# Kernel tuning notes

Hardware: AMD Instinct MI355X
Metric: run time of the kernel (lower is better)

Reference implementation:

```python
import jax, jax.numpy as jnp
import numpy as np

# Working config of MultiHeadAttention2d (see notes): B=1, k=1, n_heads=1,
# residual=True, channel_cross_attention=False, kernel_size=1.
# ConvNormActivation2d is modeled as a plain 1x1 Conv2d (bias=True for q/k/v,
# bias=False for the residual projection), i.e. identity norm/activation.
C = 64   # in_channels == out_channels == y_in == y_out (defaults, n_heads=1)
H = 36
W = 36
HW = H * W


def _conv1x1(t, Wm, b=None):
    # t: (1, C, H, W), Wm: (Cout, Cin)
    o = jnp.einsum('bchw,oc->bohw', t, Wm)
    if b is not None:
        o = o + b[None, :, None, None]
    return o


def setup_inputs() -> dict:
    key = jax.random.key(0)
    ks = jax.random.split(key, 10)
    s = 1.0 / np.sqrt(C).astype(np.float32)
    x = jax.random.normal(ks[0], (1, C, H, W), jnp.float32)
    y = jax.random.normal(ks[1], (1, C, H, W), jnp.float32)
    Wq = jax.random.normal(ks[2], (C, C), jnp.float32) * s
    bq = jnp.zeros((C,), jnp.float32)
    Wk = jax.random.normal(ks[3], (C, C), jnp.float32) * s
    bk = jnp.zeros((C,), jnp.float32)
    Wv = jax.random.normal(ks[4], (C, C), jnp.float32) * s
    bv = jnp.zeros((C,), jnp.float32)
    Wp = jax.random.normal(ks[5], (C, C), jnp.float32) * s  # residual projection, bias=False
    gamma = jax.random.uniform(ks[6], (1, 1, 1), jnp.float32) + 0.001  # torch.rand(...) + 0.001
    return {'x': x, 'y': y, 'Wq': Wq, 'bq': bq, 'Wk': Wk, 'bk': bk,
            'Wv': Wv, 'bv': bv, 'Wp': Wp, 'gamma': gamma}


def reference(x, y, Wq, bq, Wk, bk, Wv, bv, Wp, gamma):
    # 1x1-conv QKV projections
    q = _conv1x1(x, Wq, bq).reshape(C, HW)   # bmm batch dim is B*C = C (chxa=False)
    k = _conv1x1(x, Wk, bk).reshape(C, HW)
    v = _conv1x1(y, Wv, bv).reshape(C, HW)
    # energy = bmm(q^T, k) with inner dim k=1 -> per-channel outer product (C, HW, HW)
    energy = q[:, :, None] * k[:, None, :]
    att = jax.nn.softmax(energy, axis=-1)            # softmax over keys (last dim)
    # out = bmm(v, att^T): out[c,i] = sum_j v[c,j] * att[c,i,j]
    out = jnp.einsum('cij,cj->ci', att, v)           # (C, HW)
    # gamma-gated residual blend with projected y
    yproj = _conv1x1(y, Wp).reshape(C, HW)
    g = gamma.reshape(())                            # (1,1,1) gamma broadcasts as scalar
    out = (g * out + yproj) / (1.0 + g)
    return out.reshape(1, C, H, W)
```

## Files before the change

kernel.cpp:

```cpp
#include <hip/hip_runtime.h>
#include <math.h>

#define CCH 64
#define HWN 1296
#define NTHREADS 256
#define NTILES 21
#define TS 216
#define TT 6

#if defined(__has_builtin)
#  if __has_builtin(__builtin_amdgcn_exp2f)
#    define FAST_EXP2(x) __builtin_amdgcn_exp2f(x)
#  else
#    define FAST_EXP2(x) __expf((x) * 0.69314718055994531f)
#  endif
#else
#  define FAST_EXP2(x) __expf((x) * 0.69314718055994531f)
#endif

__global__ __launch_bounds__(NTHREADS) void proj2(
    const float* __restrict__ x, const float* __restrict__ y,
    const float* __restrict__ Wq, const float* __restrict__ bq,
    const float* __restrict__ Wk, const float* __restrict__ bk,
    const float* __restrict__ Wv, const float* __restrict__ bv,
    const float* __restrict__ Wp,
    float* __restrict__ q, float* __restrict__ k,
    float* __restrict__ v, float* __restrict__ yp)
{
    __shared__ float wsA[2][CCH], wsB[2][CCH];
    const int b = blockIdx.x;
    const bool xpart = (b < 324);
    const int bb = xpart ? b : b - 324;
    const int tid = threadIdx.x;
    const int idx = bb * NTHREADS + tid;
    const int c = idx / HWN;
    const int p = idx - c * HWN;
    const int c0 = (bb * NTHREADS) / HWN;
    const int c1 = (bb * NTHREADS + NTHREADS - 1) / HWN;

    {
        const int i6 = tid & 63;
        const int rsel = (tid >> 6) & 1;
        const int msel = tid >> 7;
        const int crow = rsel ? c1 : c0;
        const float* WA = xpart ? Wq : Wv;
        const float* WB = xpart ? Wk : Wp;
        if (msel == 0) wsA[rsel][i6] = WA[crow * CCH + i6];
        else           wsB[rsel][i6] = WB[crow * CCH + i6];
    }
    __syncthreads();

    const int rs = (c == c0) ? 0 : 1;
    const float* wA = wsA[rs];
    const float* wB = wsB[rs];
    float accA = xpart ? bq[c] : bv[c];
    float accB = xpart ? bk[c] : 0.f;
    const float* src = xpart ? x : y;
    const float* col = src + p;

    #pragma unroll
    for (int u = 0; u < CCH; u += 16) {
        float xv[16];
        #pragma unroll
        for (int t = 0; t < 16; ++t) xv[t] = col[(u + t) * HWN];
        #pragma unroll
        for (int t = 0; t < 16; ++t) {
            accA = fmaf(wA[u + t], xv[t], accA);
            accB = fmaf(wB[u + t], xv[t], accB);
        }
    }
    if (xpart) { q[idx] = accA; k[idx] = accB; }
    else       { v[idx] = accA; yp[idx] = accB; }
}

__global__ __launch_bounds__(NTHREADS) void att2(
    const float* __restrict__ q, const float* __restrict__ k,
    const float* __restrict__ v, const float* __restrict__ yp,
    const float* __restrict__ gamma, float* __restrict__ out)
{
    __shared__ __align__(16) float4 k4[HWN / 4];
    __shared__ __align__(16) float4 v4[HWN / 4];
    __shared__ float sse[4][64], ssev[4][64];
    __shared__ float swmax[4], swmin[4];
    const int c = blockIdx.x / NTILES;
    const int itile = blockIdx.x % NTILES;
    const int tid = threadIdx.x;
    const int w = tid >> 6;
    const int l = tid & 63;

    const float4* kg = (const float4*)(k + c * HWN);
    const float4* vg = (const float4*)(v + c * HWN);
    float lmax = -1e30f, lmin = 1e30f;
    for (int j = tid; j < HWN / 4; j += NTHREADS) {
        const float4 kk = kg[j];
        k4[j] = kk;
        v4[j] = vg[j];
        lmax = fmaxf(fmaxf(lmax, kk.x), fmaxf(kk.y, fmaxf(kk.z, kk.w)));
        lmin = fminf(fminf(lmin, kk.x), fminf(kk.y, fminf(kk.z, kk.w)));
    }
    #pragma unroll
    for (int off = 32; off > 0; off >>= 1) {
        lmax = fmaxf(lmax, __shfl_xor(lmax, off, 64));
        lmin = fminf(lmin, __shfl_xor(lmin, off, 64));
    }
    if (l == 0) { swmax[w] = lmax; swmin[w] = lmin; }
    __syncthreads();
    const float kmax = fmaxf(fmaxf(swmax[0], swmax[1]), fmaxf(swmax[2], swmax[3]));
    const float kmin = fminf(fminf(swmin[0], swmin[1]), fminf(swmin[2], swmin[3]));

    const int i = itile * 64 + l;
    const int iv = (i < HWN) ? i : (HWN - 1);
    const float L2E = 1.4426950408889634f;
    const float a2 = q[c * HWN + iv] * L2E;
    const float m2 = (a2 >= 0.f) ? a2 * kmax : a2 * kmin;
    float se = 0.f, sev = 0.f;
    const int j0 = w * 81;
    #pragma unroll 3
    for (int jj = 0; jj < 81; ++jj) {
        const float4 kk = k4[j0 + jj];
        const float4 vv = v4[j0 + jj];
        const float e0 = FAST_EXP2(fmaf(a2, kk.x, -m2));
        const float e1 = FAST_EXP2(fmaf(a2, kk.y, -m2));
        const float e2 = FAST_EXP2(fmaf(a2, kk.z, -m2));
        const float e3 = FAST_EXP2(fmaf(a2, kk.w, -m2));
        se += (e0 + e1) + (e2 + e3);
        sev = fmaf(e0, vv.x, sev);
        sev = fmaf(e1, vv.y, sev);
        sev = fmaf(e2, vv.z, sev);
        sev = fmaf(e3, vv.w, sev);
    }
    sse[w][l] = se;
    ssev[w][l] = sev;
    __syncthreads();
    if (tid < 64) {
        const int io = itile * 64 + tid;
        if (io < HWN) {
            const float seT  = (sse[0][tid] + sse[1][tid]) + (sse[2][tid] + sse[3][tid]);
            const float sevT = (ssev[0][tid] + ssev[1][tid]) + (ssev[2][tid] + ssev[3][tid]);
            const float g = gamma[0];
            out[c * HWN + io] = (g * (sevT / seT) + yp[c * HWN + io]) / (1.f + g);
        }
    }
}

__global__ __launch_bounds__(NTHREADS) void fused_kernel(
    const float* __restrict__ x, const float* __restrict__ y,
    const float* __restrict__ Wq, const float* __restrict__ bq,
    const float* __restrict__ Wk, const float* __restrict__ bk,
    const float* __restrict__ Wv, const float* __restrict__ bv,
    const float* __restrict__ Wp, const float* __restrict__ gamma,
    float* __restrict__ out)
{
    __shared__ __align__(16) float ks[HWN];
    __shared__ __align__(16) float vs[HWN];
    __shared__ float wq[CCH], wk[CCH], wv[CCH], wp[CCH];
    __shared__ float qs[TS], yps[TS];
    __shared__ float swmax[4], swmin[4];
    __shared__ float skmax, skmin;
    const int c = blockIdx.x / TT;
    const int t = blockIdx.x % TT;
    const int tid = threadIdx.x;

    if (tid < CCH) {
        wq[tid] = Wq[c * CCH + tid];
        wk[tid] = Wk[c * CCH + tid];
        wv[tid] = Wv[c * CCH + tid];
        wp[tid] = Wp[c * CCH + tid];
    }
    __syncthreads();
    const float bkc = bk[c], bvc = bv[c], bqc = bq[c];

    float lmax = -1e30f, lmin = 1e30f;
    for (int j = tid; j < HWN; j += NTHREADS) {
        float ak = bkc, av = bvc;
        #pragma unroll 8
        for (int i = 0; i < CCH; ++i) {
            ak = fmaf(wk[i], x[i * HWN + j], ak);
            av = fmaf(wv[i], y[i * HWN + j], av);
        }
        ks[j] = ak; vs[j] = av;
        lmax = fmaxf(lmax, ak);
        lmin = fminf(lmin, ak);
    }
    for (int ii = tid; ii < TS; ii += NTHREADS) {
        const int p = t * TS + ii;
        float aq = bqc, ap = 0.f;
        #pragma unroll 8
        for (int i = 0; i < CCH; ++i) {
            aq = fmaf(wq[i], x[i * HWN + p], aq);
            ap = fmaf(wp[i], y[i * HWN + p], ap);
        }
        qs[ii] = aq; yps[ii] = ap;
    }
    #pragma unroll
    for (int off = 32; off > 0; off >>= 1) {
        lmax = fmaxf(lmax, __shfl_xor(lmax, off, 64));
        lmin = fminf(lmin, __shfl_xor(lmin, off, 64));
    }
    const int wave = tid >> 6;
    if ((tid & 63) == 0) { swmax[wave] = lmax; swmin[wave] = lmin; }
    __syncthreads();
    if (tid == 0) {
        skmax = fmaxf(fmaxf(swmax[0], swmax[1]), fmaxf(swmax[2], swmax[3]));
        skmin = fminf(fminf(swmin[0], swmin[1]), fminf(swmin[2], swmin[3]));
    }
    __syncthreads();

    if (tid < TS) {
        const int i = t * TS + tid;
        const float L2E = 1.4426950408889634f;
        const float a2 = qs[tid] * L2E;
        const float m2 = (a2 >= 0.f) ? a2 * skmax : a2 * skmin;
        float se = 0.f, sev = 0.f;
        const float4* k4 = (const float4*)ks;
        const float4* v4 = (const float4*)vs;
        #pragma unroll 2
        for (int jj = 0; jj < HWN / 4; ++jj) {
            const float4 kk = k4[jj];
            const float4 vv = v4[jj];
            const float e0 = FAST_EXP2(fmaf(a2, kk.x, -m2));
            const float e1 = FAST_EXP2(fmaf(a2, kk.y, -m2));
            const float e2 = FAST_EXP2(fmaf(a2, kk.z, -m2));
            const float e3 = FAST_EXP2(fmaf(a2, kk.w, -m2));
            se += (e0 + e1) + (e2 + e3);
            sev = fmaf(e0, vv.x, sev);
            sev = fmaf(e1, vv.y, sev);
            sev = fmaf(e2, vv.z, sev);
            sev = fmaf(e3, vv.w, sev);
        }
        const float g = gamma[0];
        const float att = sev / se;
        out[c * HWN + i] = (g * att + yps[tid]) / (1.f + g);
    }
}

extern "C" void kernel_launch(void* const* d_in, const int* in_sizes, int n_in,
                              void* d_out, int out_size, void* d_ws, size_t ws_size,
                              hipStream_t stream) {
    (void)in_sizes; (void)n_in; (void)out_size;
    const float* x  = (const float*)d_in[0];
    const float* y  = (const float*)d_in[1];
    const float* Wq = (const float*)d_in[2];
    const float* bq = (const float*)d_in[3];
    const float* Wk = (const float*)d_in[4];
    const float* bk = (const float*)d_in[5];
    const float* Wv = (const float*)d_in[6];
    const float* bv = (const float*)d_in[7];
    const float* Wp = (const float*)d_in[8];
    const float* gamma = (const float*)d_in[9];
    float* out = (float*)d_out;

    const size_t need = (size_t)4 * CCH * HWN * sizeof(float);
    if (ws_size >= need) {
        float* q  = (float*)d_ws;
        float* k  = q + CCH * HWN;
        float* v  = k + CCH * HWN;
        float* yp = v + CCH * HWN;
        proj2<<<648, NTHREADS, 0, stream>>>(x, y, Wq, bq, Wk, bk, Wv, bv, Wp,
                                            q, k, v, yp);
        att2<<<CCH * NTILES, NTHREADS, 0, stream>>>(q, k, v, yp, gamma, out);
    } else {
        fused_kernel<<<CCH * TT, NTHREADS, 0, stream>>>(x, y, Wq, bq, Wk, bk, Wv, bv, Wp,
                                                        gamma, out);
    }
}
```

Measured before the change: 93.28 us.

## Process four query rows per thread in attention kernel to reuse K/V loads

The attention kernel now gives each thread up to four query positions (216-row tiles, 6 tiles per channel) instead of one per thread with 21 tiles per channel. Each LDS load of k/v float4 is reused across four rows, cutting shared-memory traffic and the per-block k/v staging and min/max reduction repeated across tiles. The cost is fewer blocks (384 vs 1344), which may hurt occupancy and load balance on the MI355X, plus 40 of 256 row slots per block do redundant work on clamped indices.

```diff
diff --git a/kernel.cpp b/kernel.cpp
--- a/kernel.cpp
+++ b/kernel.cpp
@@ -4,7 +4,9 @@
 #define CCH 64
 #define HWN 1296
 #define NTHREADS 256
-#define NTILES 21
+#define TILE_I 216
+#define NT_I 6
+#define RPL 4
 #define TS 216
 #define TT 6
 
@@ -73,20 +75,21 @@
     else       { v[idx] = accA; yp[idx] = accB; }
 }
 
-__global__ __launch_bounds__(NTHREADS) void att2(
+__global__ __launch_bounds__(NTHREADS) void att3(
     const float* __restrict__ q, const float* __restrict__ k,
     const float* __restrict__ v, const float* __restrict__ yp,
     const float* __restrict__ gamma, float* __restrict__ out)
 {
     __shared__ __align__(16) float4 k4[HWN / 4];
     __shared__ __align__(16) float4 v4[HWN / 4];
-    __shared__ float sse[4][64], ssev[4][64];
+    __shared__ float sse[4][RPL][64], ssev[4][RPL][64];
     __shared__ float swmax[4], swmin[4];
-    const int c = blockIdx.x / NTILES;
-    const int itile = blockIdx.x % NTILES;
+    const int c = blockIdx.x / NT_I;
+    const int tile = blockIdx.x % NT_I;
     const int tid = threadIdx.x;
     const int w = tid >> 6;
     const int l = tid & 63;
+    const int ibase = tile * TILE_I;
 
     const float4* kg = (const float4*)(k + c * HWN);
     const float4* vg = (const float4*)(v + c * HWN);
@@ -108,38 +111,51 @@
     const float kmax = fmaxf(fmaxf(swmax[0], swmax[1]), fmaxf(swmax[2], swmax[3]));
     const float kmin = fminf(fminf(swmin[0], swmin[1]), fminf(swmin[2], swmin[3]));
 
-    const int i = itile * 64 + l;
-    const int iv = (i < HWN) ? i : (HWN - 1);
     const float L2E = 1.4426950408889634f;
-    const float a2 = q[c * HWN + iv] * L2E;
-    const float m2 = (a2 >= 0.f) ? a2 * kmax : a2 * kmin;
-    float se = 0.f, sev = 0.f;
+    float a2[RPL], nm2[RPL];
+    #pragma unroll
+    for (int r = 0; r < RPL; ++r) {
+        int s = r * 64 + l;
+        int i = ibase + ((s < TILE_I) ? s : 0);
+        const float a = q[c * HWN + i] * L2E;
+        a2[r] = a;
+        nm2[r] = -((a >= 0.f) ? a * kmax : a * kmin);
+    }
+
+    float se[RPL], sev[RPL];
+    #pragma unroll
+    for (int r = 0; r < RPL; ++r) { se[r] = 0.f; sev[r] = 0.f; }
+
     const int j0 = w * 81;
     #pragma unroll 3
     for (int jj = 0; jj < 81; ++jj) {
         const float4 kk = k4[j0 + jj];
         const float4 vv = v4[j0 + jj];
-        const float e0 = FAST_EXP2(fmaf(a2, kk.x, -m2));
-        const float e1 = FAST_EXP2(fmaf(a2, kk.y, -m2));
-        const float e2 = FAST_EXP2(fmaf(a2, kk.z, -m2));
-        const float e3 = FAST_EXP2(fmaf(a2, kk.w, -m2));
-        se += (e0 + e1) + (e2 + e3);
-        sev = fmaf(e0, vv.x, sev);
-        sev = fmaf(e1, vv.y, sev);
-        sev = fmaf(e2, vv.z, sev);
-        sev = fmaf(e3, vv.w, sev);
-    }
-    sse[w][l] = se;
-    ssev[w][l] = sev;
-    __syncthreads();
-    if (tid < 64) {
-        const int io = itile * 64 + tid;
-        if (io < HWN) {
-            const float seT  = (sse[0][tid] + sse[1][tid]) + (sse[2][tid] + sse[3][tid]);
-            const float sevT = (ssev[0][tid] + ssev[1][tid]) + (ssev[2][tid] + ssev[3][tid]);
-            const float g = gamma[0];
-            out[c * HWN + io] = (g * (sevT / seT) + yp[c * HWN + io]) / (1.f + g);
-        }
+        #pragma unroll
+        for (int r = 0; r < RPL; ++r) {
+            const float e0 = FAST_EXP2(fmaf(a2[r], kk.x, nm2[r]));
+            const float e1 = FAST_EXP2(fmaf(a2[r], kk.y, nm2[r]));
+            const float e2 = FAST_EXP2(fmaf(a2[r], kk.z, nm2[r]));
+            const float e3 = FAST_EXP2(fmaf(a2[r], kk.w, nm2[r]));
+            se[r] += (e0 + e1) + (e2 + e3);
+            sev[r] = fmaf(e0, vv.x, sev[r]);
+            sev[r] = fmaf(e1, vv.y, sev[r]);
+            sev[r] = fmaf(e2, vv.z, sev[r]);
+            sev[r] = fmaf(e3, vv.w, sev[r]);
+        }
+    }
+    #pragma unroll
+    for (int r = 0; r < RPL; ++r) { sse[w][r][l] = se[r]; ssev[w][r][l] = sev[r]; }
+    __syncthreads();
+
+    if (tid < TILE_I) {
+        const int r = tid >> 6;
+        const int ll = tid & 63;
+        const float seT  = (sse[0][r][ll] + sse[1][r][ll]) + (sse[2][r][ll] + sse[3][r][ll]);
+        const float sevT = (ssev[0][r][ll] + ssev[1][r][ll]) + (ssev[2][r][ll] + ssev[3][r][ll]);
+        const int io = ibase + tid;
+        const float g = gamma[0];
+        out[c * HWN + io] = (g * (sevT / seT) + yp[c * HWN + io]) / (1.f + g);
     }
 }
 
@@ -258,7 +274,7 @@
         float* yp = v + CCH * HWN;
         proj2<<<648, NTHREADS, 0, stream>>>(x, y, Wq, bq, Wk, bk, Wv, bv, Wp,
                                             q, k, v, yp);
-        att2<<<CCH * NTILES, NTHREADS, 0, stream>>>(q, k, v, yp, gamma, out);
+        att3<<<CCH * NT_I, NTHREADS, 0, stream>>>(q, k, v, yp, gamma, out);
     } else {
         fused_kernel<<<CCH * TT, NTHREADS, 0, stream>>>(x, y, Wq, bq, Wk, bk, Wv, bv, Wp,
                                                         gamma, out);
```

Result: slower. 98.52 us (+5.6%).
